# Optimization experiments

Hardware: AMD Instinct MI355X
Metric: run time of the kernel (lower is better)

The kernel has to match this reference:

```python
import jax, jax.numpy as jnp
import numpy as np

NEG = -100000000.0  # NOT_POSSIBLE_TRANSITION
B, T, F, NT = 64, 512, 1024, 50
H = NT + 2  # +2 for start/stop tags
START, STOP = H - 2, H - 1


def setup_inputs() -> dict:
    key = jax.random.key(0)
    k0, k1, k2, k3 = jax.random.split(key, 4)
    features = jax.random.normal(k0, (B, T, F), jnp.float32)
    tags = jax.random.randint(k1, (B, T), 0, NT)
    masks = jnp.ones((B, T), jnp.float32)
    W = jax.random.normal(k2, (H, F), jnp.float32) * 0.02  # nn.Linear weight
    b = jnp.zeros((H,), jnp.float32)                        # nn.Linear bias
    transition = jax.random.normal(k3, (H, H), jnp.float32)
    transition = transition.at[START, :].set(NEG).at[:, STOP].set(NEG)
    return dict(features=features, W=W, b=b, transition=transition,
                masks=masks, tags=tags)


def _forward_algorithm(emit, masks, transition):
    # emit: [B,T,H], masks: [B,T]
    b_, _, h = emit.shape
    init = jnp.full((b_, h), NEG, emit.dtype).at[:, START].set(0.0)

    def step(scores, xs):
        emit_t, mask_t = xs  # [B,H], [B]
        # score_t[b, i] = logsumexp_j(scores[b,j] + transition[i,j] + emit_t[b,i])
        s = scores[:, None, :] + transition[None, :, :] + emit_t[:, :, None]
        s = jax.nn.logsumexp(s, axis=-1)
        m = mask_t[:, None]
        scores = s * m + scores * (1.0 - m)
        return scores, None

    scores, _ = jax.lax.scan(step, init, (emit.transpose(1, 0, 2), masks.T))
    return jax.nn.logsumexp(scores + transition[STOP], axis=-1)  # [B]


def _gold_score(emit, tags, masks, transition):
    b_ = emit.shape[0]
    emit_sc = jnp.take_along_axis(emit, tags[:, :, None], axis=2)[:, :, 0]  # [B,T]
    start = jnp.full((b_, 1), START, tags.dtype)
    tags_ext = jnp.concatenate([start, tags], axis=1)  # [B,T+1]
    trans_sc = transition[tags_ext[:, 1:], tags_ext[:, :-1]]  # [B,T]
    last_pos = masks.sum(axis=1).astype(jnp.int32)  # index into tags_ext
    last_tag = jnp.take_along_axis(tags_ext, last_pos[:, None], axis=1)[:, 0]
    last_score = transition[STOP, last_tag]
    return ((trans_sc + emit_sc) * masks).sum(axis=1) + last_score  # [B]


def reference(features, W, b, transition, masks, tags):
    emit = features @ W.T + b  # [B,T,H]
    fwd = _forward_algorithm(emit, masks, transition)
    gold = _gold_score(emit, tags, masks, transition)
    return (fwd - gold).mean()  # CRF NLL loss (scalar)


if __name__ == "__main__":
    print(reference(**setup_inputs()))
```

## Files before the change

kernel.cpp:

```cpp
#include <hip/hip_runtime.h>
#include <hip/hip_bf16.h>
#include <math.h>


#define NEGV   (-100000000.0f)
#define BB     64
#define TT     512
#define FF     1024
#define HH     52
#define HP     64
#define S_START 50
#define S_STOP  51
#define NCH    32
#define CLEN   (TT / NCH)

typedef __bf16 bf16x8 __attribute__((ext_vector_type(8)));
typedef __bf16 bf16x4 __attribute__((ext_vector_type(4)));
typedef float  f32x4  __attribute__((ext_vector_type(4)));

#define WS_CHUNK  0u
#define WS_EMITB  16777216u
#define WS_WBF    20971520u
#define WS_EXPT   21102592u
#define WS_GOLD   21110784u
#define WS_CEXP   21111040u

__global__ __launch_bounds__(256) void k_prep(const float* __restrict__ W,
                                              const float* __restrict__ trans,
                                              __bf16* __restrict__ wbf,
                                              __bf16* __restrict__ expT,
                                              float* __restrict__ gold) {
  int n = blockIdx.x;
  if (n == 0) {
    if (threadIdx.x < BB) gold[threadIdx.x] = 0.0f;
    for (int idx = threadIdx.x; idx < 4096; idx += 256) {
      int m = idx >> 6, k = idx & 63;
      float tv = (k >= HH) ? NEGV : ((m >= HH) ? 0.0f : trans[m * HH + k]);
      expT[idx] = (__bf16)__expf(tv);
    }
  }
  for (int k = threadIdx.x; k < FF; k += 256) {
    float v = (n < HH) ? W[n * FF + k] : 0.0f;
    wbf[n * FF + k] = (__bf16)v;
  }
}

__global__ __launch_bounds__(256, 2) void k_emit(const float* __restrict__ feat,
                                                 const __bf16* __restrict__ wbf,
                                                 const float* __restrict__ bias,
                                                 __bf16* __restrict__ emitb) {
  const int tid = threadIdx.x;
  const int wv = tid >> 6;
  const int l  = tid & 63;
  const int lm = l & 15;
  const int q  = l >> 4;
  const size_t row0 = (size_t)blockIdx.x * 64 + wv * 16;
  const float* arow = feat + (row0 + lm) * FF + q * 8;

  float bn[4];
#pragma unroll
  for (int nt = 0; nt < 4; ++nt) {
    int n = nt * 16 + lm;
    bn[nt] = (n < HH) ? bias[n] : 0.0f;
  }

  f32x4 apre[4][2];
#pragma unroll
  for (int s = 0; s < 4; ++s)
#pragma unroll
    for (int h = 0; h < 2; ++h)
      apre[s][h] = *(const f32x4*)(arow + s * 32 + h * 4);

  bf16x8 bpre[2][4];
#pragma unroll
  for (int sb = 0; sb < 2; ++sb)
#pragma unroll
    for (int nt = 0; nt < 4; ++nt)
      bpre[sb][nt] = *(const bf16x8*)(wbf + (size_t)(nt * 16 + lm) * FF + sb * 32 + q * 8);

  f32x4 acc[4] = {};

#pragma unroll
  for (int kt = 0; kt < 32; ++kt) {
    const int st = kt & 3, sb = kt & 1;
    bf16x8 af;
#pragma unroll
    for (int j = 0; j < 4; ++j) {
      af[j]     = (__bf16)apre[st][0][j];
      af[4 + j] = (__bf16)apre[st][1][j];
    }
#pragma unroll
    for (int nt = 0; nt < 4; ++nt)
      acc[nt] = __builtin_amdgcn_mfma_f32_16x16x32_bf16(af, bpre[sb][nt], acc[nt], 0, 0, 0);
    if (kt + 4 < 32) {
#pragma unroll
      for (int h = 0; h < 2; ++h)
        apre[st][h] = *(const f32x4*)(arow + (kt + 4) * 32 + h * 4);
    }
    if (kt + 2 < 32) {
#pragma unroll
      for (int nt = 0; nt < 4; ++nt)
        bpre[sb][nt] = *(const bf16x8*)(wbf + (size_t)(nt * 16 + lm) * FF + (kt + 2) * 32 + q * 8);
    }
  }

#pragma unroll
  for (int nt = 0; nt < 4; ++nt)
#pragma unroll
    for (int rr = 0; rr < 4; ++rr)
      emitb[(row0 + q * 4 + rr) * HP + nt * 16 + lm] = (__bf16)(acc[nt][rr] + bn[nt]);
}

__global__ __launch_bounds__(256, 2) void k_scan(const __bf16* __restrict__ emitb,
                                                 const __bf16* __restrict__ expT,
                                                 const float* __restrict__ trans,
                                                 const float* __restrict__ masks,
                                                 const int* __restrict__ tags,
                                                 __bf16* __restrict__ chunks,
                                                 float* __restrict__ cexp,
                                                 float* __restrict__ gold) {
  const int tid = threadIdx.x;
  const int wv = tid >> 6;
  const int l  = tid & 63;
  const int lm = l & 15;
  const int q  = l >> 4;
  const int chunk = blockIdx.x * 4 + wv;
  const int b = chunk >> 5, c = chunk & 31;

  __shared__ __align__(16) __bf16 PTall[4][64 * 72];
  __shared__ __align__(16) float  Eall[4][CLEN * 64];
  __bf16* pt = PTall[wv];
  float*  E  = Eall[wv];

  const float LOG2E = 1.4426950408889634f;
  const float LN2   = 0.6931471805599453f;

  const __bf16* tb = emitb + (size_t)(b * TT + c * CLEN) * HP;
  bf16x8 v0 = *(const bf16x8*)(tb + l * 16);
  bf16x8 v1 = *(const bf16x8*)(tb + l * 16 + 8);
  float ev[16];
#pragma unroll
  for (int j = 0; j < 8; ++j) {
    ev[j]     = __builtin_amdgcn_exp2f(fmaf((float)v0[j], LOG2E, -7.0f));
    ev[8 + j] = __builtin_amdgcn_exp2f(fmaf((float)v1[j], LOG2E, -7.0f));
  }
#pragma unroll
  for (int h = 0; h < 4; ++h) {
    f32x4 e4 = { ev[h * 4], ev[h * 4 + 1], ev[h * 4 + 2], ev[h * 4 + 3] };
    *(f32x4*)&E[l * 16 + h * 4] = e4;
  }

  bf16x8 afrag[4][2];
#pragma unroll
  for (int mt = 0; mt < 4; ++mt)
#pragma unroll
    for (int kk = 0; kk < 2; ++kk)
      afrag[mt][kk] = *(const bf16x8*)&expT[(mt * 16 + lm) * 64 + kk * 32 + q * 8];

  for (int idx = l; idx < 4096; idx += 64) {
    int n = idx >> 6, mm = idx & 63;
    pt[n * 72 + mm] = (__bf16)((n == mm) ? 1.0f : 0.0f);
  }

  float mreg = (l < CLEN) ? masks[b * TT + c * CLEN + l] : 1.0f;
  int cur = (l < CLEN) ? tags[b * TT + c * CLEN + l] : 0;
  int prev = __shfl_up(cur, 1);
  if (l == 0) prev = (c == 0) ? S_START : tags[b * TT + c * CLEN - 1];
  float gp = 0.0f;
  if (l < CLEN) {
    float e = fmaf(__log2f(E[l * 64 + cur]), LN2, 7.0f * LN2);
    gp = (e + trans[cur * HH + prev]) * mreg;
  }
#pragma unroll
  for (int d = 1; d < 64; d <<= 1) gp += __shfl_xor(gp, d);
  if (l == 0) atomicAdd(&gold[b], gp);

  int eacc = 0, rpend = 0;
  float rs = 1.0f;

  for (int t = 0; t < CLEN; ++t) {
    float mcur = __shfl(mreg, t);
    if (mcur != 0.0f) {
      eacc += 7 + rpend;
      float s[4][4];
#pragma unroll
      for (int mt = 0; mt < 4; ++mt) {
        f32x4 e4 = *(const f32x4*)&E[t * 64 + mt * 16 + q * 4];
#pragma unroll
        for (int rr = 0; rr < 4; ++rr) s[mt][rr] = e4[rr] * rs;
      }

      bf16x8 bfr[2][4];
#pragma unroll
      for (int kk = 0; kk < 2; ++kk)
#pragma unroll
        for (int nt = 0; nt < 4; ++nt)
          bfr[kk][nt] = *(const bf16x8*)&pt[(nt * 16 + lm) * 72 + kk * 32 + q * 8];

      const bool trk = (t == 7);
      float lmax = 0.0f;
      f32x4 zero = {};
#pragma unroll
      for (int mt = 0; mt < 4; ++mt) {
#pragma unroll
        for (int nt = 0; nt < 4; ++nt) {
          f32x4 a = __builtin_amdgcn_mfma_f32_16x16x32_bf16(afrag[mt][0], bfr[0][nt], zero, 0, 0, 0);
          a = __builtin_amdgcn_mfma_f32_16x16x32_bf16(afrag[mt][1], bfr[1][nt], a, 0, 0, 0);
          bf16x4 w4;
#pragma unroll
          for (int rr = 0; rr < 4; ++rr) {
            float v = a[rr] * s[mt][rr];
            if (trk) lmax = fmaxf(lmax, v);
            w4[rr] = (__bf16)v;
          }
          *(bf16x4*)&pt[(nt * 16 + lm) * 72 + mt * 16 + q * 4] = w4;
        }
      }
      if (trk) {
#pragma unroll
        for (int d = 1; d < 64; d <<= 1) lmax = fmaxf(lmax, __shfl_xor(lmax, d));
        rpend = ilogbf(lmax);
        rs = __builtin_amdgcn_exp2f(-(float)rpend);
      } else {
        rpend = 0;
        rs = 1.0f;
      }
    }
  }

  __bf16* cb = chunks + (size_t)chunk * 4096;
#pragma unroll
  for (int jj = 0; jj < 8; ++jj) {
    bf16x8 w;
#pragma unroll
    for (int e = 0; e < 8; ++e) w[e] = pt[(jj * 8 + e) * 72 + l];
    *(bf16x8*)(cb + jj * 512 + l * 8) = w;
  }
  if (l == 0) cexp[chunk] = (float)eacc;
}

__global__ __launch_bounds__(64) void k_combine(const __bf16* __restrict__ chunks,
                                                const float* __restrict__ cexp,
                                                const float* __restrict__ trans,
                                                const float* __restrict__ masks,
                                                const int* __restrict__ tags,
                                                const float* __restrict__ gold,
                                                float* __restrict__ out) {
  const int b = blockIdx.x;
  const int l = threadIdx.x;
  __shared__ float vsh[64];
  float v = (l == S_START) ? 1.0f : 0.0f;
  float esum = 0.0f;
  const float LN2 = 0.6931471805599453f;

  float msum = 0.0f;
  for (int t = l; t < TT; t += 64) msum += masks[b * TT + t];

  bf16x8 mb[2][8];
  {
    const __bf16* base = chunks + (size_t)(b * NCH) * 4096;
#pragma unroll
    for (int jj = 0; jj < 8; ++jj) mb[0][jj] = *(const bf16x8*)(base + jj * 512 + l * 8);
  }

#pragma unroll
  for (int cc = 0; cc < NCH; ++cc) {
    vsh[l] = v;
    __syncthreads();
    if (cc + 1 < NCH) {
      const __bf16* bn = chunks + (size_t)(b * NCH + cc + 1) * 4096;
#pragma unroll
      for (int jj = 0; jj < 8; ++jj) mb[(cc + 1) & 1][jj] = *(const bf16x8*)(bn + jj * 512 + l * 8);
    }
    float u0 = 0.f, u1 = 0.f;
#pragma unroll
    for (int jj = 0; jj < 8; ++jj) {
      bf16x8 m8 = mb[cc & 1][jj];
      const float* vj = &vsh[jj * 8];
#pragma unroll
      for (int e = 0; e < 4; ++e) {
        u0 += (float)m8[e] * vj[e];
        u1 += (float)m8[4 + e] * vj[4 + e];
      }
    }
    float u = u0 + u1;
    esum += cexp[b * NCH + cc] * LN2;
    float mxx = u;
#pragma unroll
    for (int d = 1; d < 64; d <<= 1) mxx = fmaxf(mxx, __shfl_xor(mxx, d));
    if (mxx > 0.0f) {
      int ee = ilogbf(mxx);
      u = ldexpf(u, -ee);
      esum += (float)ee * LN2;
    }
    v = u;
    __syncthreads();
  }

  float ts = (l < HH) ? trans[S_STOP * HH + l] : NEGV;
  float contrib = v * __expf(ts);
#pragma unroll
  for (int d = 1; d < 64; d <<= 1) {
    contrib += __shfl_xor(contrib, d);
    msum += __shfl_xor(msum, d);
  }
  if (l == 0) {
    int lp = (int)(msum + 0.5f);
    int lt = (lp == 0) ? S_START : tags[b * TT + lp - 1];
    float goldb = gold[b] + trans[S_STOP * HH + lt];
    float fwd = __logf(contrib) + esum;
    atomicAdd(out, (fwd - goldb) * (1.0f / 64.0f));
  }
}

extern "C" void kernel_launch(void* const* d_in, const int* in_sizes, int n_in,
                              void* d_out, int out_size, void* d_ws, size_t ws_size,
                              hipStream_t stream) {
  (void)in_sizes; (void)n_in; (void)out_size; (void)ws_size;
  const float* feat  = (const float*)d_in[0];
  const float* W     = (const float*)d_in[1];
  const float* bias  = (const float*)d_in[2];
  const float* trans = (const float*)d_in[3];
  const float* masks = (const float*)d_in[4];
  const int*   tags  = (const int*)d_in[5];

  char* ws = (char*)d_ws;
  __bf16* chunks = (__bf16*)(ws + WS_CHUNK);
  __bf16* emitb  = (__bf16*)(ws + WS_EMITB);
  __bf16* wbf    = (__bf16*)(ws + WS_WBF);
  __bf16* expT   = (__bf16*)(ws + WS_EXPT);
  float*  gold   = (float*)(ws + WS_GOLD);
  float*  cexp   = (float*)(ws + WS_CEXP);

  hipMemsetAsync(d_out, 0, sizeof(float), stream);
  k_prep<<<HP, 256, 0, stream>>>(W, trans, wbf, expT, gold);
  k_emit<<<(BB * TT) / 64, 256, 0, stream>>>(feat, wbf, bias, emitb);
  k_scan<<<(BB * NCH) / 4, 256, 0, stream>>>(emitb, expT, trans, masks, tags,
                                             chunks, cexp, gold);
  k_combine<<<BB, 64, 0, stream>>>(chunks, cexp, trans, masks, tags, gold, (float*)d_out);
}
```

Baseline: 284.5 us.

## Fuse emission GEMM into chunked scan kernel and double chunk count

Removes the separate emission kernel and its bf16 intermediate buffer: each scan wavefront now computes its own chunk's emissions with MFMA directly from the features, exponentiates them, and keeps them in shared memory as bf16. The chunk count is doubled so each chunk covers 8 timesteps, which drops the mid-chunk rescaling logic and increases parallelism, but the combine kernel must now walk twice as many chunk matrices serially. Half the MFMA rows are wasted because 8 time rows are duplicated into 16, and storing exponentiated emissions in bf16 reduces precision.

After: 355.1 us. +24.8%, slower.

```diff
diff --git a/kernel.cpp b/kernel.cpp
--- a/kernel.cpp
+++ b/kernel.cpp
@@ -11,7 +11,7 @@
 #define HP     64
 #define S_START 50
 #define S_STOP  51
-#define NCH    32
+#define NCH    64
 #define CLEN   (TT / NCH)
 
 typedef __bf16 bf16x8 __attribute__((ext_vector_type(8)));
@@ -19,11 +19,10 @@
 typedef float  f32x4  __attribute__((ext_vector_type(4)));
 
 #define WS_CHUNK  0u
-#define WS_EMITB  16777216u
-#define WS_WBF    20971520u
-#define WS_EXPT   21102592u
-#define WS_GOLD   21110784u
-#define WS_CEXP   21111040u
+#define WS_WBF    33554432u
+#define WS_EXPT   33685504u
+#define WS_GOLD   33693696u
+#define WS_CEXP   33693952u
 
 __global__ __launch_bounds__(256) void k_prep(const float* __restrict__ W,
                                               const float* __restrict__ trans,
@@ -45,74 +44,10 @@
   }
 }
 
-__global__ __launch_bounds__(256, 2) void k_emit(const float* __restrict__ feat,
+__global__ __launch_bounds__(256, 4) void k_scan(const float* __restrict__ feat,
                                                  const __bf16* __restrict__ wbf,
+                                                 const __bf16* __restrict__ expT,
                                                  const float* __restrict__ bias,
-                                                 __bf16* __restrict__ emitb) {
-  const int tid = threadIdx.x;
-  const int wv = tid >> 6;
-  const int l  = tid & 63;
-  const int lm = l & 15;
-  const int q  = l >> 4;
-  const size_t row0 = (size_t)blockIdx.x * 64 + wv * 16;
-  const float* arow = feat + (row0 + lm) * FF + q * 8;
-
-  float bn[4];
-#pragma unroll
-  for (int nt = 0; nt < 4; ++nt) {
-    int n = nt * 16 + lm;
-    bn[nt] = (n < HH) ? bias[n] : 0.0f;
-  }
-
-  f32x4 apre[4][2];
-#pragma unroll
-  for (int s = 0; s < 4; ++s)
-#pragma unroll
-    for (int h = 0; h < 2; ++h)
-      apre[s][h] = *(const f32x4*)(arow + s * 32 + h * 4);
-
-  bf16x8 bpre[2][4];
-#pragma unroll
-  for (int sb = 0; sb < 2; ++sb)
-#pragma unroll
-    for (int nt = 0; nt < 4; ++nt)
-      bpre[sb][nt] = *(const bf16x8*)(wbf + (size_t)(nt * 16 + lm) * FF + sb * 32 + q * 8);
-
-  f32x4 acc[4] = {};
-
-#pragma unroll
-  for (int kt = 0; kt < 32; ++kt) {
-    const int st = kt & 3, sb = kt & 1;
-    bf16x8 af;
-#pragma unroll
-    for (int j = 0; j < 4; ++j) {
-      af[j]     = (__bf16)apre[st][0][j];
-      af[4 + j] = (__bf16)apre[st][1][j];
-    }
-#pragma unroll
-    for (int nt = 0; nt < 4; ++nt)
-      acc[nt] = __builtin_amdgcn_mfma_f32_16x16x32_bf16(af, bpre[sb][nt], acc[nt], 0, 0, 0);
-    if (kt + 4 < 32) {
-#pragma unroll
-      for (int h = 0; h < 2; ++h)
-        apre[st][h] = *(const f32x4*)(arow + (kt + 4) * 32 + h * 4);
-    }
-    if (kt + 2 < 32) {
-#pragma unroll
-      for (int nt = 0; nt < 4; ++nt)
-        bpre[sb][nt] = *(const bf16x8*)(wbf + (size_t)(nt * 16 + lm) * FF + (kt + 2) * 32 + q * 8);
-    }
-  }
-
-#pragma unroll
-  for (int nt = 0; nt < 4; ++nt)
-#pragma unroll
-    for (int rr = 0; rr < 4; ++rr)
-      emitb[(row0 + q * 4 + rr) * HP + nt * 16 + lm] = (__bf16)(acc[nt][rr] + bn[nt]);
-}
-
-__global__ __launch_bounds__(256, 2) void k_scan(const __bf16* __restrict__ emitb,
-                                                 const __bf16* __restrict__ expT,
                                                  const float* __restrict__ trans,
                                                  const float* __restrict__ masks,
                                                  const int* __restrict__ tags,
@@ -125,41 +60,66 @@
   const int lm = l & 15;
   const int q  = l >> 4;
   const int chunk = blockIdx.x * 4 + wv;
-  const int b = chunk >> 5, c = chunk & 31;
+  const int b = chunk >> 6, c = chunk & 63;
 
   __shared__ __align__(16) __bf16 PTall[4][64 * 72];
-  __shared__ __align__(16) float  Eall[4][CLEN * 64];
-  __bf16* pt = PTall[wv];
-  float*  E  = Eall[wv];
-
+  __shared__ __align__(16) __bf16 ELall[4][CLEN * 64];
   const float LOG2E = 1.4426950408889634f;
   const float LN2   = 0.6931471805599453f;
 
-  const __bf16* tb = emitb + (size_t)(b * TT + c * CLEN) * HP;
-  bf16x8 v0 = *(const bf16x8*)(tb + l * 16);
-  bf16x8 v1 = *(const bf16x8*)(tb + l * 16 + 8);
-  float ev[16];
-#pragma unroll
-  for (int j = 0; j < 8; ++j) {
-    ev[j]     = __builtin_amdgcn_exp2f(fmaf((float)v0[j], LOG2E, -7.0f));
-    ev[8 + j] = __builtin_amdgcn_exp2f(fmaf((float)v1[j], LOG2E, -7.0f));
-  }
-#pragma unroll
-  for (int h = 0; h < 4; ++h) {
-    f32x4 e4 = { ev[h * 4], ev[h * 4 + 1], ev[h * 4 + 2], ev[h * 4 + 3] };
-    *(f32x4*)&E[l * 16 + h * 4] = e4;
-  }
-
-  bf16x8 afrag[4][2];
-#pragma unroll
-  for (int mt = 0; mt < 4; ++mt)
-#pragma unroll
-    for (int kk = 0; kk < 2; ++kk)
-      afrag[mt][kk] = *(const bf16x8*)&expT[(mt * 16 + lm) * 64 + kk * 32 + q * 8];
-
-  for (int idx = l; idx < 4096; idx += 64) {
-    int n = idx >> 6, mm = idx & 63;
-    pt[n * 72 + mm] = (__bf16)((n == mm) ? 1.0f : 0.0f);
+  const float* arow = feat + ((size_t)(b * TT + c * CLEN) + (lm & 7)) * FF + q * 8;
+
+  f32x4 apre[4][2];
+#pragma unroll
+  for (int s = 0; s < 4; ++s)
+#pragma unroll
+    for (int h = 0; h < 2; ++h)
+      apre[s][h] = *(const f32x4*)(arow + s * 32 + h * 4);
+
+  bf16x8 bpre[2][4];
+#pragma unroll
+  for (int sb = 0; sb < 2; ++sb)
+#pragma unroll
+    for (int nt = 0; nt < 4; ++nt)
+      bpre[sb][nt] = *(const bf16x8*)(wbf + (size_t)(nt * 16 + lm) * FF + sb * 32 + q * 8);
+
+  f32x4 acc[4] = {};
+
+#pragma unroll
+  for (int kt = 0; kt < 32; ++kt) {
+    const int st = kt & 3, sb = kt & 1;
+    bf16x8 af;
+#pragma unroll
+    for (int j = 0; j < 4; ++j) {
+      af[j]     = (__bf16)apre[st][0][j];
+      af[4 + j] = (__bf16)apre[st][1][j];
+    }
+#pragma unroll
+    for (int nt = 0; nt < 4; ++nt)
+      acc[nt] = __builtin_amdgcn_mfma_f32_16x16x32_bf16(af, bpre[sb][nt], acc[nt], 0, 0, 0);
+    if (kt + 4 < 32) {
+#pragma unroll
+      for (int h = 0; h < 2; ++h)
+        apre[st][h] = *(const f32x4*)(arow + (kt + 4) * 32 + h * 4);
+    }
+    if (kt + 2 < 32) {
+#pragma unroll
+      for (int nt = 0; nt < 4; ++nt)
+        bpre[sb][nt] = *(const bf16x8*)(wbf + (size_t)(nt * 16 + lm) * FF + (kt + 2) * 32 + q * 8);
+    }
+  }
+
+  if (q < 2) {
+#pragma unroll
+    for (int nt = 0; nt < 4; ++nt) {
+      int n = nt * 16 + lm;
+      float bn = (n < HH) ? bias[n] : 0.0f;
+#pragma unroll
+      for (int rr = 0; rr < 4; ++rr) {
+        float e = acc[nt][rr] + bn;
+        ELall[wv][(q * 4 + rr) * 64 + n] = (__bf16)__builtin_amdgcn_exp2f(fmaf(e, LOG2E, -7.0f));
+      }
+    }
   }
 
   float mreg = (l < CLEN) ? masks[b * TT + c * CLEN + l] : 1.0f;
@@ -168,26 +128,37 @@
   if (l == 0) prev = (c == 0) ? S_START : tags[b * TT + c * CLEN - 1];
   float gp = 0.0f;
   if (l < CLEN) {
-    float e = fmaf(__log2f(E[l * 64 + cur]), LN2, 7.0f * LN2);
+    float e = fmaf(__log2f((float)ELall[wv][l * 64 + cur]), LN2, 7.0f * LN2);
     gp = (e + trans[cur * HH + prev]) * mreg;
   }
 #pragma unroll
   for (int d = 1; d < 64; d <<= 1) gp += __shfl_xor(gp, d);
   if (l == 0) atomicAdd(&gold[b], gp);
 
-  int eacc = 0, rpend = 0;
-  float rs = 1.0f;
-
+  bf16x8 afrag[4][2];
+#pragma unroll
+  for (int mt = 0; mt < 4; ++mt)
+#pragma unroll
+    for (int kk = 0; kk < 2; ++kk)
+      afrag[mt][kk] = *(const bf16x8*)&expT[(mt * 16 + lm) * 64 + kk * 32 + q * 8];
+
+#pragma unroll
+  for (int i = 0; i < 64; ++i)
+    PTall[wv][i * 72 + l] = (__bf16)((i == l) ? 1.0f : 0.0f);
+
+  int eacc = 0;
+
+#pragma unroll
   for (int t = 0; t < CLEN; ++t) {
     float mcur = __shfl(mreg, t);
     if (mcur != 0.0f) {
-      eacc += 7 + rpend;
+      eacc += 7;
       float s[4][4];
 #pragma unroll
       for (int mt = 0; mt < 4; ++mt) {
-        f32x4 e4 = *(const f32x4*)&E[t * 64 + mt * 16 + q * 4];
-#pragma unroll
-        for (int rr = 0; rr < 4; ++rr) s[mt][rr] = e4[rr] * rs;
+        bf16x4 e4 = *(const bf16x4*)&ELall[wv][t * 64 + mt * 16 + q * 4];
+#pragma unroll
+        for (int rr = 0; rr < 4; ++rr) s[mt][rr] = (float)e4[rr];
       }
 
       bf16x8 bfr[2][4];
@@ -195,10 +166,8 @@
       for (int kk = 0; kk < 2; ++kk)
 #pragma unroll
         for (int nt = 0; nt < 4; ++nt)
-          bfr[kk][nt] = *(const bf16x8*)&pt[(nt * 16 + lm) * 72 + kk * 32 + q * 8];
-
-      const bool trk = (t == 7);
-      float lmax = 0.0f;
+          bfr[kk][nt] = *(const bf16x8*)&PTall[wv][(nt * 16 + lm) * 72 + kk * 32 + q * 8];
+
       f32x4 zero = {};
 #pragma unroll
       for (int mt = 0; mt < 4; ++mt) {
@@ -208,22 +177,9 @@
           a = __builtin_amdgcn_mfma_f32_16x16x32_bf16(afrag[mt][1], bfr[1][nt], a, 0, 0, 0);
           bf16x4 w4;
 #pragma unroll
-          for (int rr = 0; rr < 4; ++rr) {
-            float v = a[rr] * s[mt][rr];
-            if (trk) lmax = fmaxf(lmax, v);
-            w4[rr] = (__bf16)v;
-          }
-          *(bf16x4*)&pt[(nt * 16 + lm) * 72 + mt * 16 + q * 4] = w4;
+          for (int rr = 0; rr < 4; ++rr) w4[rr] = (__bf16)(a[rr] * s[mt][rr]);
+          *(bf16x4*)&PTall[wv][(nt * 16 + lm) * 72 + mt * 16 + q * 4] = w4;
         }
-      }
-      if (trk) {
-#pragma unroll
-        for (int d = 1; d < 64; d <<= 1) lmax = fmaxf(lmax, __shfl_xor(lmax, d));
-        rpend = ilogbf(lmax);
-        rs = __builtin_amdgcn_exp2f(-(float)rpend);
-      } else {
-        rpend = 0;
-        rs = 1.0f;
       }
     }
   }
@@ -233,7 +189,7 @@
   for (int jj = 0; jj < 8; ++jj) {
     bf16x8 w;
 #pragma unroll
-    for (int e = 0; e < 8; ++e) w[e] = pt[(jj * 8 + e) * 72 + l];
+    for (int e = 0; e < 8; ++e) w[e] = PTall[wv][(jj * 8 + e) * 72 + l];
     *(bf16x8*)(cb + jj * 512 + l * 8) = w;
   }
   if (l == 0) cexp[chunk] = (float)eacc;
@@ -263,7 +219,6 @@
     for (int jj = 0; jj < 8; ++jj) mb[0][jj] = *(const bf16x8*)(base + jj * 512 + l * 8);
   }
 
-#pragma unroll
   for (int cc = 0; cc < NCH; ++cc) {
     vsh[l] = v;
     __syncthreads();
@@ -326,7 +281,6 @@
 
   char* ws = (char*)d_ws;
   __bf16* chunks = (__bf16*)(ws + WS_CHUNK);
-  __bf16* emitb  = (__bf16*)(ws + WS_EMITB);
   __bf16* wbf    = (__bf16*)(ws + WS_WBF);
   __bf16* expT   = (__bf16*)(ws + WS_EXPT);
   float*  gold   = (float*)(ws + WS_GOLD);
@@ -334,8 +288,7 @@
 
   hipMemsetAsync(d_out, 0, sizeof(float), stream);
   k_prep<<<HP, 256, 0, stream>>>(W, trans, wbf, expT, gold);
-  k_emit<<<(BB * TT) / 64, 256, 0, stream>>>(feat, wbf, bias, emitb);
-  k_scan<<<(BB * NCH) / 4, 256, 0, stream>>>(emitb, expT, trans, masks, tags,
-                                             chunks, cexp, gold);
+  k_scan<<<(BB * NCH) / 4, 256, 0, stream>>>(feat, wbf, expT, bias, trans, masks,
+                                             tags, chunks, cexp, gold);
   k_combine<<<BB, 64, 0, stream>>>(chunks, cexp, trans, masks, tags, gold, (float*)d_out);
 }
```
